# Kernel optimization log

Hardware: AMD Instinct MI355X
Metric: run time of the kernel (lower is better)

Reference implementation:

```python
import jax, jax.numpy as jnp
import numpy as np

N_CODES = 1024
CODE_DIM = 64
COMMITMENT_WEIGHT = 0.5
DECAY = 0.99
EPSILON = 1e-05
TEMP = 1.0


def setup_inputs() -> dict:
    key = jax.random.key(0)
    k_z, k_e = jax.random.split(key)
    z = jax.random.normal(k_z, (8, 16384, CODE_DIM), dtype=jnp.float32)
    # xavier_uniform init for embedding [n_codes, code_dim]
    limit = float(np.sqrt(6.0 / (N_CODES + CODE_DIM)))
    embedding = jax.random.uniform(k_e, (N_CODES, CODE_DIM), dtype=jnp.float32,
                                   minval=-limit, maxval=limit)
    ema_cluster_size = jnp.zeros((N_CODES,), dtype=jnp.float32)
    ema_w = embedding.copy()
    return {"z": z, "embedding": embedding,
            "ema_cluster_size": ema_cluster_size, "ema_w": ema_w}


def reference(z, embedding, ema_cluster_size, ema_w):
    lead_shape = z.shape[:-1]
    zf = z.reshape(-1, z.shape[-1])  # [N, D]
    # squared-euclidean distances: ||z||^2 + ||e||^2 - 2 z e^T  -> [N, n_codes]
    d = (jnp.sum(zf * zf, axis=-1, keepdims=True)
         + jnp.sum(embedding * embedding, axis=-1)
         - 2.0 * (zf @ embedding.T)) / TEMP
    idx = jnp.argmin(d, axis=-1)  # [N]
    z_q_f = embedding[idx]        # [N, D]

    # --- EMA codebook update (no-grad buffer math) ---
    ones = jnp.ones_like(idx, dtype=zf.dtype)
    cluster_size = jax.ops.segment_sum(ones, idx, num_segments=N_CODES)      # one_hot.sum(0)
    new_ecs = ema_cluster_size * DECAY + (1.0 - DECAY) * cluster_size
    n = jnp.sum(new_ecs)
    cs = jnp.clip((new_ecs + EPSILON) / (n + N_CODES * EPSILON) * n, 0.01)
    dw = jax.ops.segment_sum(zf, idx, num_segments=N_CODES)                  # one_hot.T @ z
    new_ema_w = ema_w * DECAY + (1.0 - DECAY) * dw
    new_embedding = new_ema_w / cs[:, None]

    # --- losses (straight-through) ---
    z_q = z_q_f.reshape(z.shape)
    commitment_loss = jnp.mean((jax.lax.stop_gradient(z_q) - z) ** 2)
    codebook_loss = jnp.mean((z_q - jax.lax.stop_gradient(z)) ** 2)
    loss = commitment_loss * COMMITMENT_WEIGHT + codebook_loss
    z_q_st = z + jax.lax.stop_gradient(z_q - z)

    # --- perplexity (no-grad) ---
    avg_probs = cluster_size / jnp.sum(cluster_size)
    avg_probs = jnp.clip(avg_probs, 1e-10)
    avg_probs = avg_probs / jnp.sum(avg_probs)
    perplexity = jnp.exp(-jnp.sum(avg_probs * jnp.log(avg_probs)))

    encoding_indices = idx.reshape(lead_shape)
    return (z_q_st, encoding_indices, loss, perplexity,
            new_embedding, new_ecs, new_ema_w)
```

## Files before the change

### kernel.cpp

```cpp
#include <hip/hip_runtime.h>
#include <hip/hip_bf16.h>
#include <math.h>

#define N_ROWS   131072
#define DIMS     64
#define NCODES   1024
#define DECAY    0.99f
#define EPSF     1e-5f
#define BAND     2e-3f

#define OFF_ZQ    0
#define OFF_IDX   8388608
#define OFF_LOSS  8519680
#define OFF_PERP  8519681
#define OFF_EMB   8519682
#define OFF_ECS   8585218
#define OFF_EMAW  8586242

typedef unsigned int uint;
typedef short bf16x8 __attribute__((ext_vector_type(8)));
typedef float f32x4  __attribute__((ext_vector_type(4)));

__device__ __forceinline__ float atomic_add_f32(float* p, float v) {
  return __hip_atomic_fetch_add(p, v, __ATOMIC_RELAXED, __HIP_MEMORY_SCOPE_AGENT);
}

__device__ __forceinline__ unsigned short bf16_rne(float f) {
  uint u = __float_as_uint(f);
  uint r = u + 0x7fffu + ((u >> 16) & 1u);
  return (unsigned short)(r >> 16);
}
__device__ __forceinline__ float bf16_f32(unsigned short h) {
  return __uint_as_float(((uint)h) << 16);
}

__device__ __forceinline__ float np_pairwise64_sq(const float* v) {
#pragma clang fp contract(off)
  float r[8];
#pragma unroll
  for (int j = 0; j < 8; ++j) r[j] = v[j] * v[j];
#pragma unroll
  for (int i = 8; i < 64; i += 8)
#pragma unroll
    for (int j = 0; j < 8; ++j) r[j] += v[i + j] * v[i + j];
  return ((r[0] + r[1]) + (r[2] + r[3])) + ((r[4] + r[5]) + (r[6] + r[7]));
}

__global__ __launch_bounds__(256) void k0m(const float* __restrict__ emb,
                                           float* __restrict__ ee,
                                           uint* __restrict__ cluster,
                                           uint* __restrict__ cnt,
                                           bf16x8* __restrict__ bsplit,
                                           float* __restrict__ dw) {
  int T = blockIdx.x;
  int t = threadIdx.x;
  int gid = T * 256 + t;
  for (int i = gid; i < NCODES * DIMS; i += 16384) dw[i] = 0.0f;

  int l = t & 63;
  int slot = t >> 6;
  int ktile = slot >> 1, split = slot & 1;
  int code = T * 16 + (l & 15);
  int k0 = ktile * 32 + ((l >> 4) << 3);
  const float* ep = emb + (size_t)code * DIMS + k0;
  float4 fa = *(const float4*)ep;
  float4 fb = *(const float4*)(ep + 4);
  float fs[8] = {fa.x, fa.y, fa.z, fa.w, fb.x, fb.y, fb.z, fb.w};
  bf16x8 v;
#pragma unroll
  for (int i = 0; i < 8; ++i) {
    unsigned short h = bf16_rne(fs[i]);
    if (split == 0) v[i] = (short)h;
    else            v[i] = (short)bf16_rne(fs[i] - bf16_f32(h));
  }
  bsplit[(size_t)((T * 2 + ktile) * 2 + split) * 64 + l] = v;

  if (t < 16) {
    int c = T * 16 + t;
    float ev[DIMS];
    const float4* e4 = (const float4*)(emb + (size_t)c * DIMS);
#pragma unroll
    for (int i = 0; i < 16; ++i) {
      float4 w = e4[i];
      ev[4*i] = w.x; ev[4*i+1] = w.y; ev[4*i+2] = w.z; ev[4*i+3] = w.w;
    }
    ee[c] = np_pairwise64_sq(ev);
  } else if (t < 32) {
    cluster[T * 16 + (t - 16)] = 0u;
  }
  if (T == 0 && t == 32) *cnt = 0u;
}

__global__ __launch_bounds__(256) void k1_mfma(const float* __restrict__ z,
                                               const float* __restrict__ emb,
                                               const bf16x8* __restrict__ bsplit,
                                               const float* __restrict__ ee,
                                               int* __restrict__ idx_out,
                                               float* __restrict__ idx_f_out,
                                               float* __restrict__ out_zq,
                                               double* __restrict__ sqpart,
                                               uint* __restrict__ cluster,
                                               uint* __restrict__ cnt,
                                               uint* __restrict__ list) {
  __shared__ bf16x8 btile[2][256];
  __shared__ float  eel[NCODES];
  __shared__ int    sidx[64];
  __shared__ double wred[4];
  int t = threadIdx.x;
  int l = t & 63;
  int w = t >> 6;
  int rowbase = blockIdx.x * 64 + w * 16;
  int arow = rowbase + (l & 15);
  int kq = (l >> 4) << 3;
  int col = l & 15;

  for (int i = t; i < NCODES; i += 256) eel[i] = ee[i];

  bf16x8 ahi[2], ami[2];
#pragma unroll
  for (int t2 = 0; t2 < 2; ++t2) {
    const float* zp = z + (size_t)arow * DIMS + t2 * 32 + kq;
    float4 fa = *(const float4*)zp;
    float4 fb = *(const float4*)(zp + 4);
    float fs[8] = {fa.x, fa.y, fa.z, fa.w, fb.x, fb.y, fb.z, fb.w};
#pragma unroll
    for (int i = 0; i < 8; ++i) {
      unsigned short h = bf16_rne(fs[i]);
      float m = fs[i] - bf16_f32(h);
      ahi[t2][i] = (short)bf16_rne(-2.0f * fs[i]);
      ami[t2][i] = (short)bf16_rne(-2.0f * m);
    }
  }

  float best[4]  = {3.4e38f, 3.4e38f, 3.4e38f, 3.4e38f};
  float second[4] = {3.4e38f, 3.4e38f, 3.4e38f, 3.4e38f};
  int   bidx[4] = {0, 0, 0, 0};

  bf16x8 vp0 = bsplit[(size_t)(0 * 4 + w) * 64 + l];
  bf16x8 vp1 = bsplit[(size_t)(1 * 4 + w) * 64 + l];

  for (int T = 0; T < 64; T += 2) {
    __syncthreads();
    btile[0][w * 64 + l] = vp0;
    btile[1][w * 64 + l] = vp1;
    __syncthreads();
    if (T + 2 < 64) {
      vp0 = bsplit[(size_t)((T + 2) * 4 + w) * 64 + l];
      vp1 = bsplit[(size_t)((T + 3) * 4 + w) * 64 + l];
    }

#pragma unroll
    for (int u = 0; u < 2; ++u) {
      int code = (T + u) * 16 + col;
      float eeT = eel[code];
      bf16x8 bhi0 = btile[u][0 * 64 + l];
      bf16x8 bmi0 = btile[u][1 * 64 + l];
      bf16x8 bhi1 = btile[u][2 * 64 + l];
      bf16x8 bmi1 = btile[u][3 * 64 + l];

      f32x4 acc = {eeT, eeT, eeT, eeT};
      acc = __builtin_amdgcn_mfma_f32_16x16x32_bf16(ahi[0], bhi0, acc, 0, 0, 0);
      acc = __builtin_amdgcn_mfma_f32_16x16x32_bf16(ahi[1], bhi1, acc, 0, 0, 0);
      acc = __builtin_amdgcn_mfma_f32_16x16x32_bf16(ahi[0], bmi0, acc, 0, 0, 0);
      acc = __builtin_amdgcn_mfma_f32_16x16x32_bf16(ahi[1], bmi1, acc, 0, 0, 0);
      acc = __builtin_amdgcn_mfma_f32_16x16x32_bf16(ami[0], bhi0, acc, 0, 0, 0);
      acc = __builtin_amdgcn_mfma_f32_16x16x32_bf16(ami[1], bhi1, acc, 0, 0, 0);

#pragma unroll
      for (int j = 0; j < 4; ++j) {
        float s = acc[j];
        bool lt = s < best[j];
        second[j] = lt ? best[j] : fminf(second[j], s);
        best[j]   = lt ? s : best[j];
        bidx[j]   = lt ? code : bidx[j];
      }
    }
  }

#pragma unroll
  for (int m = 1; m < 16; m <<= 1) {
#pragma unroll
    for (int j = 0; j < 4; ++j) {
      float ob = __shfl_xor(best[j], m, 64);
      float os = __shfl_xor(second[j], m, 64);
      int   oi = __shfl_xor(bidx[j], m, 64);
      if (ob < best[j]) {
        second[j] = fminf(os, best[j]);
        best[j] = ob; bidx[j] = oi;
      } else if (ob == best[j]) {
        bidx[j] = min(bidx[j], oi);
        second[j] = fminf(second[j], fminf(os, ob));
      } else {
        second[j] = fminf(second[j], ob);
      }
    }
  }

  if (col == 0) {
#pragma unroll
    for (int j = 0; j < 4; ++j) {
      int lrow = w * 16 + ((l >> 4) << 2) + j;
      int r = blockIdx.x * 64 + lrow;
      sidx[lrow] = bidx[j];
      idx_out[r] = bidx[j];
      idx_f_out[r] = (float)bidx[j];
      atomicAdd(&cluster[bidx[j]], 1u);
      if (second[j] - best[j] < BAND) {
        uint p = atomicAdd(cnt, 1u);
        list[p] = (uint)r;
      }
    }
  }
  __syncthreads();

  double ds = 0.0;
  const float4* z4 = (const float4*)z;
  const float4* e4 = (const float4*)emb;
  float4* zq4 = (float4*)out_zq;
  int blockrow = blockIdx.x * 64;
#pragma unroll
  for (int p = 0; p < 4; ++p) {
    int f = t + p * 256;
    int lrow = f >> 4, d4 = f & 15;
    int code = sidx[lrow];
    float4 zv = z4[(size_t)(blockrow + lrow) * 16 + d4];
    float4 ev = e4[code * 16 + d4];
    float dx = ev.x - zv.x, dy = ev.y - zv.y, dz = ev.z - zv.z, dw_ = ev.w - zv.w;
    float4 o;
    o.x = zv.x + dx; o.y = zv.y + dy; o.z = zv.z + dz; o.w = zv.w + dw_;
    zq4[(size_t)(blockrow + lrow) * 16 + d4] = o;
    float ss = dx * dx + dy * dy + dz * dz + dw_ * dw_;
    ds += (double)ss;
  }
#pragma unroll
  for (int o2 = 32; o2 > 0; o2 >>= 1) ds += __shfl_down(ds, o2, 64);
  if (l == 0) wred[w] = ds;
  __syncthreads();
  if (t == 0) sqpart[blockIdx.x] = (wred[0] + wred[1]) + (wred[2] + wred[3]);
}

__global__ __launch_bounds__(256) void k2_recheck(const float* __restrict__ z,
                                                  const float* __restrict__ emb,
                                                  const float* __restrict__ ee,
                                                  const uint* __restrict__ cnt,
                                                  const uint* __restrict__ list,
                                                  int* __restrict__ idx_out,
                                                  float* __restrict__ idx_f_out,
                                                  float* __restrict__ out_zq,
                                                  uint* __restrict__ cluster,
                                                  double* __restrict__ corr) {
#pragma clang fp contract(off)
  __shared__ float zrow[DIMS];
  __shared__ float rv[256];
  __shared__ int   ri[256];
  __shared__ int   schg, sold, snew;
  int t = threadIdx.x;
  uint n = *cnt;
  double corrAcc = 0.0;
  const float4* e4 = (const float4*)emb;
  float4* zq4 = (float4*)out_zq;

  for (uint i = blockIdx.x; i < n; i += gridDim.x) {
    uint row = list[i];
    __syncthreads();
    if (t < 16)
      ((float4*)zrow)[t] = ((const float4*)(z + (size_t)row * DIMS))[t];
    __syncthreads();
    float zz = np_pairwise64_sq(zrow);
    float best = 3.4e38f; int bi = 0;
#pragma unroll
    for (int k4 = 0; k4 < 4; ++k4) {
      int c = t * 4 + k4;
      const float* e = emb + (size_t)c * DIMS;
      float a = 0.f;
      for (int k = 0; k < DIMS; ++k) a = fmaf(zrow[k], e[k], a);
      float d = fmaf(-2.0f, a, zz + ee[c]);
      if (d < best) { best = d; bi = c; }
    }
    rv[t] = best; ri[t] = bi;
    __syncthreads();
    for (int s = 128; s > 0; s >>= 1) {
      if (t < s) {
        float ov = rv[t + s]; int oi = ri[t + s];
        if (ov < rv[t] || (ov == rv[t] && oi < ri[t])) { rv[t] = ov; ri[t] = oi; }
      }
      __syncthreads();
    }
    if (t == 0) {
      int old = idx_out[row];
      if (ri[0] != old) {
        atomicSub(&cluster[old], 1u);
        atomicAdd(&cluster[ri[0]], 1u);
        idx_out[row] = ri[0];
        idx_f_out[row] = (float)ri[0];
        schg = 1; sold = old; snew = ri[0];
      } else {
        schg = 0;
      }
    }
    __syncthreads();
    if (schg && t < 16) {
      float4 zv = make_float4(zrow[t*4], zrow[t*4+1], zrow[t*4+2], zrow[t*4+3]);
      float4 en = e4[snew * 16 + t];
      float4 eo = e4[sold * 16 + t];
      float dxn = en.x - zv.x, dyn = en.y - zv.y, dzn = en.z - zv.z, dwn = en.w - zv.w;
      float4 o;
      o.x = zv.x + dxn; o.y = zv.y + dyn; o.z = zv.z + dzn; o.w = zv.w + dwn;
      zq4[(size_t)row * 16 + t] = o;
      float ssn = dxn * dxn + dyn * dyn + dzn * dzn + dwn * dwn;
      float dxo = eo.x - zv.x, dyo = eo.y - zv.y, dzo = eo.z - zv.z, dwo = eo.w - zv.w;
      float sso = dxo * dxo + dyo * dyo + dzo * dzo + dwo * dwo;
      double cl = (double)ssn - (double)sso;
      cl += __shfl_xor(cl, 1, 64);
      cl += __shfl_xor(cl, 2, 64);
      cl += __shfl_xor(cl, 4, 64);
      cl += __shfl_xor(cl, 8, 64);
      if (t == 0) corrAcc += cl;
    }
  }
  if (t == 0) corr[blockIdx.x] = corrAcc;
}

__global__ __launch_bounds__(256) void kp(const uint* __restrict__ cluster,
                                          const float* __restrict__ ecs_in,
                                          uint* __restrict__ starts,
                                          uint* __restrict__ cursor,
                                          float* __restrict__ csb,
                                          float* __restrict__ out) {
  __shared__ uint a[256], b[256];
  __shared__ double red[256];
  int t = threadIdx.x;

  uint c0 = cluster[t*4+0], c1 = cluster[t*4+1], c2 = cluster[t*4+2], c3 = cluster[t*4+3];
  uint s4 = c0 + c1 + c2 + c3;
  a[t] = s4;
  __syncthreads();
  uint* src = a; uint* dst = b;
  for (int off = 1; off < 256; off <<= 1) {
    dst[t] = src[t] + ((t >= off) ? src[t - off] : 0u);
    __syncthreads();
    uint* tmp = src; src = dst; dst = tmp;
  }
  uint base = (t > 0) ? src[t-1] : 0u;
  uint p0 = base, p1 = p0 + c0, p2 = p1 + c1, p3 = p2 + c2;
  starts[t*4+0] = p0; starts[t*4+1] = p1; starts[t*4+2] = p2; starts[t*4+3] = p3;
  cursor[t*4+0] = p0; cursor[t*4+1] = p1; cursor[t*4+2] = p2; cursor[t*4+3] = p3;
  if (t == 255) starts[NCODES] = src[255];
  __syncthreads();

  double nloc = 0.0, aloc = 0.0, bloc = 0.0;
  for (int c = t; c < NCODES; c += 256) {
    float cntf = (float)cluster[c];
    float ne = ecs_in[c] * DECAY + (1.0f - DECAY) * cntf;
    out[OFF_ECS + c] = ne;
    nloc += (double)ne;
    double p = (double)cntf / (double)N_ROWS;
    double pc = p < 1e-10 ? 1e-10 : p;
    bloc += pc;
    aloc += pc * log(pc);
  }

  red[t] = nloc; __syncthreads();
  for (int s = 128; s > 0; s >>= 1) { if (t < s) red[t] += red[t + s]; __syncthreads(); }
  double n = red[0]; __syncthreads();

  red[t] = bloc; __syncthreads();
  for (int s = 128; s > 0; s >>= 1) { if (t < s) red[t] += red[t + s]; __syncthreads(); }
  double B = red[0]; __syncthreads();

  red[t] = aloc; __syncthreads();
  for (int s = 128; s > 0; s >>= 1) { if (t < s) red[t] += red[t + s]; __syncthreads(); }
  double A = red[0]; __syncthreads();

  if (t == 0) {
    double ent = -(A / B - log(B));
    out[OFF_PERP] = (float)exp(ent);
  }

  float nf = (float)n;
  for (int c = t; c < NCODES; c += 256) {
    float ne = out[OFF_ECS + c];
    float cs = ((ne + EPSF) / (nf + (float)NCODES * EPSF)) * nf;
    csb[c] = cs < 0.01f ? 0.01f : cs;
  }
}

__global__ __launch_bounds__(256) void k3c_scatter(const int* __restrict__ idx,
                                                   uint* __restrict__ cursor,
                                                   uint* __restrict__ rowids,
                                                   int* __restrict__ codes) {
  int row = blockIdx.x * 256 + threadIdx.x;
  int code = idx[row];
  uint pos = atomicAdd(&cursor[code], 1u);
  rowids[pos] = (uint)row;
  codes[pos] = code;
}

__global__ __launch_bounds__(256) void k3d_dw(const float* __restrict__ z,
                                              const uint* __restrict__ rowids,
                                              const int* __restrict__ codes,
                                              float* __restrict__ dw) {
  int lane = threadIdx.x & 63, w = threadIdx.x >> 6;
  int base = blockIdx.x * 128 + w * 32;

  int cur = codes[base];
  float acc = 0.f;
  for (int i = 0; i < 32; ++i) {
    int p = base + i;
    uint r = rowids[p];
    int c = codes[p];
    if (c != cur) {
      atomic_add_f32(&dw[cur * DIMS + lane], acc);
      acc = 0.f; cur = c;
    }
    acc += z[(size_t)r * DIMS + lane];
  }
  atomic_add_f32(&dw[cur * DIMS + lane], acc);
}

__global__ __launch_bounds__(256) void k4b_emb(const float* __restrict__ emaw_in,
                                               const float* __restrict__ dw,
                                               const float* __restrict__ csb,
                                               const double* __restrict__ sqpart,
                                               const double* __restrict__ corr,
                                               float* __restrict__ out) {
  int i = blockIdx.x * 256 + threadIdx.x;
  int c = i >> 6;
  float nw = emaw_in[i] * DECAY + (1.0f - DECAY) * dw[i];
  out[OFF_EMAW + i] = nw;
  out[OFF_EMB + i] = nw / csb[c];

  if (blockIdx.x == 0) {
    __shared__ double red[256];
    int t = threadIdx.x;
    double sloc = 0.0;
    for (int k = t; k < 2048; k += 256) sloc += sqpart[k];
    for (int k = t; k < 1024; k += 256) sloc += corr[k];
    red[t] = sloc; __syncthreads();
    for (int s = 128; s > 0; s >>= 1) { if (t < s) red[t] += red[t + s]; __syncthreads(); }
    if (t == 0) {
      double M = red[0] / (double)((size_t)N_ROWS * DIMS);
      out[OFF_LOSS] = (float)(1.5 * M);
    }
  }
}

extern "C" void kernel_launch(void* const* d_in, const int* in_sizes, int n_in,
                              void* d_out, int out_size, void* d_ws, size_t ws_size,
                              hipStream_t stream) {
  const float* z    = (const float*)d_in[0];
  const float* emb  = (const float*)d_in[1];
  const float* ecs  = (const float*)d_in[2];
  const float* emaw = (const float*)d_in[3];
  float* out = (float*)d_out;

  char* ws = (char*)d_ws;
  uint*   cnt    = (uint*)   (ws + 0);
  int*    idxw   = (int*)    (ws + 16);
  uint*   clus   = (uint*)   (ws + 524304);
  float*  dw     = (float*)  (ws + 528416);
  float*  ee     = (float*)  (ws + 790560);
  float*  csb    = (float*)  (ws + 794656);
  uint*   starts = (uint*)   (ws + 798752);
  uint*   cursor = (uint*)   (ws + 806944);
  uint*   rowids = (uint*)   (ws + 811040);
  bf16x8* bsplit = (bf16x8*) (ws + 1335328);
  uint*   rlist  = (uint*)   (ws + 1597472);
  int*    codes  = (int*)    (ws + 2121760);
  double* sqpart = (double*) (ws + 2646048);
  double* corr   = (double*) (ws + 2662432);

  k0m<<<64, 256, 0, stream>>>(emb, ee, clus, cnt, bsplit, dw);
  k1_mfma<<<N_ROWS / 64, 256, 0, stream>>>(z, emb, bsplit, ee, idxw,
                                           out + OFF_IDX, out + OFF_ZQ,
                                           sqpart, clus, cnt, rlist);
  k2_recheck<<<1024, 256, 0, stream>>>(z, emb, ee, cnt, rlist, idxw,
                                       out + OFF_IDX, out + OFF_ZQ, clus, corr);
  kp<<<1, 256, 0, stream>>>(clus, ecs, starts, cursor, csb, out);
  k3c_scatter<<<N_ROWS / 256, 256, 0, stream>>>(idxw, cursor, rowids, codes);
  k3d_dw<<<N_ROWS / 128, 256, 0, stream>>>(z, rowids, codes, dw);
  k4b_emb<<<256, 256, 0, stream>>>(emaw, dw, csb, sqpart, corr, out);
}
```

Baseline: 191.3 us.

## Fuse dw segment-sum into distance kernel via direct float atomics

```diff
diff --git a/kernel.cpp b/kernel.cpp
--- a/kernel.cpp
+++ b/kernel.cpp
@@ -21,8 +21,8 @@
 typedef short bf16x8 __attribute__((ext_vector_type(8)));
 typedef float f32x4  __attribute__((ext_vector_type(4)));
 
-__device__ __forceinline__ float atomic_add_f32(float* p, float v) {
-  return __hip_atomic_fetch_add(p, v, __ATOMIC_RELAXED, __HIP_MEMORY_SCOPE_AGENT);
+__device__ __forceinline__ void atomic_add_f32_nr(float* p, float v) {
+  __hip_atomic_fetch_add(p, v, __ATOMIC_RELAXED, __HIP_MEMORY_SCOPE_AGENT);
 }
 
 __device__ __forceinline__ unsigned short bf16_rne(float f) {
@@ -100,6 +100,7 @@
                                                float* __restrict__ out_zq,
                                                double* __restrict__ sqpart,
                                                uint* __restrict__ cluster,
+                                               float* __restrict__ dw,
                                                uint* __restrict__ cnt,
                                                uint* __restrict__ list) {
   __shared__ bf16x8 btile[2][256];
@@ -231,6 +232,11 @@
     zq4[(size_t)(blockrow + lrow) * 16 + d4] = o;
     float ss = dx * dx + dy * dy + dz * dz + dw_ * dw_;
     ds += (double)ss;
+    float* dwp = dw + (size_t)code * DIMS + d4 * 4;
+    atomic_add_f32_nr(dwp + 0, zv.x);
+    atomic_add_f32_nr(dwp + 1, zv.y);
+    atomic_add_f32_nr(dwp + 2, zv.z);
+    atomic_add_f32_nr(dwp + 3, zv.w);
   }
 #pragma unroll
   for (int o2 = 32; o2 > 0; o2 >>= 1) ds += __shfl_down(ds, o2, 64);
@@ -248,6 +254,7 @@
                                                   float* __restrict__ idx_f_out,
                                                   float* __restrict__ out_zq,
                                                   uint* __restrict__ cluster,
+                                                  float* __restrict__ dw,
                                                   double* __restrict__ corr) {
 #pragma clang fp contract(off)
   __shared__ float zrow[DIMS];
@@ -307,9 +314,15 @@
       float4 o;
       o.x = zv.x + dxn; o.y = zv.y + dyn; o.z = zv.z + dzn; o.w = zv.w + dwn;
       zq4[(size_t)row * 16 + t] = o;
+      float* dwo = dw + (size_t)sold * DIMS + t * 4;
+      float* dwn2 = dw + (size_t)snew * DIMS + t * 4;
+      atomic_add_f32_nr(dwo + 0, -zv.x); atomic_add_f32_nr(dwn2 + 0, zv.x);
+      atomic_add_f32_nr(dwo + 1, -zv.y); atomic_add_f32_nr(dwn2 + 1, zv.y);
+      atomic_add_f32_nr(dwo + 2, -zv.z); atomic_add_f32_nr(dwn2 + 2, zv.z);
+      atomic_add_f32_nr(dwo + 3, -zv.w); atomic_add_f32_nr(dwn2 + 3, zv.w);
       float ssn = dxn * dxn + dyn * dyn + dzn * dzn + dwn * dwn;
-      float dxo = eo.x - zv.x, dyo = eo.y - zv.y, dzo = eo.z - zv.z, dwo = eo.w - zv.w;
-      float sso = dxo * dxo + dyo * dyo + dzo * dzo + dwo * dwo;
+      float dxo = eo.x - zv.x, dyo = eo.y - zv.y, dzo = eo.z - zv.z, dwo2 = eo.w - zv.w;
+      float sso = dxo * dxo + dyo * dyo + dzo * dzo + dwo2 * dwo2;
       double cl = (double)ssn - (double)sso;
       cl += __shfl_xor(cl, 1, 64);
       cl += __shfl_xor(cl, 2, 64);
@@ -323,30 +336,10 @@
 
 __global__ __launch_bounds__(256) void kp(const uint* __restrict__ cluster,
                                           const float* __restrict__ ecs_in,
-                                          uint* __restrict__ starts,
-                                          uint* __restrict__ cursor,
                                           float* __restrict__ csb,
                                           float* __restrict__ out) {
-  __shared__ uint a[256], b[256];
   __shared__ double red[256];
   int t = threadIdx.x;
-
-  uint c0 = cluster[t*4+0], c1 = cluster[t*4+1], c2 = cluster[t*4+2], c3 = cluster[t*4+3];
-  uint s4 = c0 + c1 + c2 + c3;
-  a[t] = s4;
-  __syncthreads();
-  uint* src = a; uint* dst = b;
-  for (int off = 1; off < 256; off <<= 1) {
-    dst[t] = src[t] + ((t >= off) ? src[t - off] : 0u);
-    __syncthreads();
-    uint* tmp = src; src = dst; dst = tmp;
-  }
-  uint base = (t > 0) ? src[t-1] : 0u;
-  uint p0 = base, p1 = p0 + c0, p2 = p1 + c1, p3 = p2 + c2;
-  starts[t*4+0] = p0; starts[t*4+1] = p1; starts[t*4+2] = p2; starts[t*4+3] = p3;
-  cursor[t*4+0] = p0; cursor[t*4+1] = p1; cursor[t*4+2] = p2; cursor[t*4+3] = p3;
-  if (t == 255) starts[NCODES] = src[255];
-  __syncthreads();
 
   double nloc = 0.0, aloc = 0.0, bloc = 0.0;
   for (int c = t; c < NCODES; c += 256) {
@@ -383,39 +376,6 @@
     float cs = ((ne + EPSF) / (nf + (float)NCODES * EPSF)) * nf;
     csb[c] = cs < 0.01f ? 0.01f : cs;
   }
-}
-
-__global__ __launch_bounds__(256) void k3c_scatter(const int* __restrict__ idx,
-                                                   uint* __restrict__ cursor,
-                                                   uint* __restrict__ rowids,
-                                                   int* __restrict__ codes) {
-  int row = blockIdx.x * 256 + threadIdx.x;
-  int code = idx[row];
-  uint pos = atomicAdd(&cursor[code], 1u);
-  rowids[pos] = (uint)row;
-  codes[pos] = code;
-}
-
-__global__ __launch_bounds__(256) void k3d_dw(const float* __restrict__ z,
-                                              const uint* __restrict__ rowids,
-                                              const int* __restrict__ codes,
-                                              float* __restrict__ dw) {
-  int lane = threadIdx.x & 63, w = threadIdx.x >> 6;
-  int base = blockIdx.x * 128 + w * 32;
-
-  int cur = codes[base];
-  float acc = 0.f;
-  for (int i = 0; i < 32; ++i) {
-    int p = base + i;
-    uint r = rowids[p];
-    int c = codes[p];
-    if (c != cur) {
-      atomic_add_f32(&dw[cur * DIMS + lane], acc);
-      acc = 0.f; cur = c;
-    }
-    acc += z[(size_t)r * DIMS + lane];
-  }
-  atomic_add_f32(&dw[cur * DIMS + lane], acc);
 }
 
 __global__ __launch_bounds__(256) void k4b_emb(const float* __restrict__ emaw_in,
@@ -461,23 +421,18 @@
   float*  dw     = (float*)  (ws + 528416);
   float*  ee     = (float*)  (ws + 790560);
   float*  csb    = (float*)  (ws + 794656);
-  uint*   starts = (uint*)   (ws + 798752);
-  uint*   cursor = (uint*)   (ws + 806944);
-  uint*   rowids = (uint*)   (ws + 811040);
   bf16x8* bsplit = (bf16x8*) (ws + 1335328);
   uint*   rlist  = (uint*)   (ws + 1597472);
-  int*    codes  = (int*)    (ws + 2121760);
   double* sqpart = (double*) (ws + 2646048);
   double* corr   = (double*) (ws + 2662432);
 
   k0m<<<64, 256, 0, stream>>>(emb, ee, clus, cnt, bsplit, dw);
   k1_mfma<<<N_ROWS / 64, 256, 0, stream>>>(z, emb, bsplit, ee, idxw,
                                            out + OFF_IDX, out + OFF_ZQ,
-                                           sqpart, clus, cnt, rlist);
+                                           sqpart, clus, dw, cnt, rlist);
   k2_recheck<<<1024, 256, 0, stream>>>(z, emb, ee, cnt, rlist, idxw,
-                                       out + OFF_IDX, out + OFF_ZQ, clus, corr);
-  kp<<<1, 256, 0, stream>>>(clus, ecs, starts, cursor, csb, out);
-  k3c_scatter<<<N_ROWS / 256, 256, 0, stream>>>(idxw, cursor, rowids, codes);
-  k3d_dw<<<N_ROWS / 128, 256, 0, stream>>>(z, rowids, codes, dw);
+                                       out + OFF_IDX, out + OFF_ZQ, clus, dw,
+                                       corr);
+  kp<<<1, 256, 0, stream>>>(clus, ecs, csb, out);
   k4b_emb<<<256, 256, 0, stream>>>(emaw, dw, csb, sqpart, corr, out);
 }
```

Measured after the change: 288.2 us. 1.51x slower.
